# Optimization experiments

Hardware: AMD Instinct MI355X
Metric: run time of the kernel (lower is better)

## Reference

```python
import jax, jax.numpy as jnp
import numpy as np

B, S, H, NH = 8, 1024, 768, 12
I = 3072
HD = H // NH  # 64


def setup_inputs() -> dict:
    key = jax.random.key(0)
    ks = jax.random.split(key, 6)
    w = lambda k, shape: jax.random.normal(k, shape, jnp.float32) * 0.02
    return {
        "x": jax.random.normal(ks[0], (B, S, H), jnp.float32),
        "ln1_g": jnp.ones((H,), jnp.float32),
        "ln1_b": jnp.zeros((H,), jnp.float32),
        "qkv_w": w(ks[1], (H, 3 * H)),
        "qkv_b": jnp.zeros((3 * H,), jnp.float32),
        "proj_w": w(ks[2], (H, H)),
        "proj_b": jnp.zeros((H,), jnp.float32),
        "ln2_g": jnp.ones((H,), jnp.float32),
        "ln2_b": jnp.zeros((H,), jnp.float32),
        "fc1_w": w(ks[3], (H, I)),
        "fc1_b": jnp.zeros((I,), jnp.float32),
        "fc2_w": w(ks[4], (I, H)),
        "fc2_b": jnp.zeros((H,), jnp.float32),
    }


def _layernorm(x, g, b, eps=1e-5):
    m = x.mean(-1, keepdims=True)
    v = x.var(-1, keepdims=True)  # biased variance, matches torch LayerNorm
    return (x - m) * jax.lax.rsqrt(v + eps) * g + b


def _new_gelu(x):
    c = np.float32(np.sqrt(2.0 / np.pi))
    return 0.5 * x * (1.0 + jnp.tanh(c * (x + 0.044715 * x * x * x)))


def reference(x, ln1_g, ln1_b, qkv_w, qkv_b, proj_w, proj_b,
              ln2_g, ln2_b, fc1_w, fc1_b, fc2_w, fc2_b):
    # --- attention sublayer (pre-LN) ---
    h = _layernorm(x, ln1_g, ln1_b)                     # [B,S,H]
    qkv = h @ qkv_w + qkv_b                             # [B,S,3H]
    q, k, v = jnp.split(qkv, 3, axis=-1)
    q = q.reshape(B, S, NH, HD).transpose(0, 2, 1, 3)   # [B,NH,S,HD]
    k = k.reshape(B, S, NH, HD).transpose(0, 2, 1, 3)
    v = v.reshape(B, S, NH, HD).transpose(0, 2, 1, 3)
    scores = jnp.einsum('bhtd,bhsd->bhts', q, k) / np.float32(np.sqrt(HD))
    probs = jax.nn.softmax(scores, axis=-1)             # [B,NH,S,S]
    attn = jnp.einsum('bhts,bhsd->bhtd', probs, v)      # [B,NH,S,HD]
    attn = attn.transpose(0, 2, 1, 3).reshape(B, S, H)
    attn = attn @ proj_w + proj_b
    x = x + attn
    # --- MLP sublayer (pre-LN) ---
    h2 = _layernorm(x, ln2_g, ln2_b)
    m = _new_gelu(h2 @ fc1_w + fc1_b) @ fc2_w + fc2_b
    return x + m
```

## Files before the change

kernel.cpp:

```cpp
#include <hip/hip_runtime.h>
#include <hip/hip_bf16.h>


typedef __attribute__((ext_vector_type(8))) short bf16x8;
typedef __attribute__((ext_vector_type(4))) float f32x4;
typedef const __attribute__((address_space(3))) char* lds_cp;

#define MFMA16(a, b, c) __builtin_amdgcn_mfma_f32_16x16x32_bf16((a), (b), (c), 0, 0, 0)

#define DSR(dst, addr, off) \
    asm volatile("ds_read_b128 %0, %1 offset:" #off : "=v"(dst) : "v"(addr))
#define WAITV4 asm volatile("s_waitcnt vmcnt(4)" ::: "memory")
#define WAITV0 asm volatile("s_waitcnt vmcnt(0)" ::: "memory")
#define WAITLG asm volatile("s_waitcnt lgkmcnt(0)" ::: "memory")
#define SCHEDB __builtin_amdgcn_sched_barrier(0)

__device__ inline short f2bf(float x) {
    __hip_bfloat16 h = __float2bfloat16(x);
    return *reinterpret_cast<short*>(&h);
}

__device__ inline void gload_lds16(const void* g, void* lds) {
    __builtin_amdgcn_global_load_lds(
        (const __attribute__((address_space(1))) unsigned int*)g,
        (__attribute__((address_space(3))) unsigned int*)lds,
        16, 0, 0);
}

__global__ __launch_bounds__(256) void transpose_w(
    const float* __restrict__ W, short* __restrict__ Wt, int K, int N) {
    __shared__ float tile[32][33];
    const int tx = threadIdx.x & 31, ty = threadIdx.x >> 5;
    const int n0 = blockIdx.x * 32, k0 = blockIdx.y * 32;
#pragma unroll
    for (int i = 0; i < 4; ++i)
        tile[ty + i * 8][tx] = W[(size_t)(k0 + ty + i * 8) * N + n0 + tx];
    __syncthreads();
#pragma unroll
    for (int i = 0; i < 4; ++i)
        Wt[(size_t)(n0 + ty + i * 8) * K + k0 + tx] = f2bf(tile[tx][ty + i * 8]);
}

__global__ __launch_bounds__(256) void ln_k(
    const float* __restrict__ x, const float* __restrict__ g,
    const float* __restrict__ b, short* __restrict__ out) {
    const int row = blockIdx.x;
    const int tid = threadIdx.x;
    const float* xr = x + (size_t)row * 768;
    float v[3];
    float s = 0.f, sq = 0.f;
#pragma unroll
    for (int i = 0; i < 3; ++i) {
        v[i] = xr[tid + i * 256];
        s += v[i];
        sq += v[i] * v[i];
    }
#pragma unroll
    for (int off = 32; off >= 1; off >>= 1) {
        s += __shfl_xor(s, off);
        sq += __shfl_xor(sq, off);
    }
    __shared__ float ss[4], ssq[4];
    const int wid = tid >> 6;
    if ((tid & 63) == 0) { ss[wid] = s; ssq[wid] = sq; }
    __syncthreads();
    s = ss[0] + ss[1] + ss[2] + ss[3];
    sq = ssq[0] + ssq[1] + ssq[2] + ssq[3];
    const float mean = s * (1.0f / 768.0f);
    const float var = sq * (1.0f / 768.0f) - mean * mean;
    const float rstd = rsqrtf(var + 1e-5f);
    short* outr = out + (size_t)row * 768;
#pragma unroll
    for (int i = 0; i < 3; ++i) {
        const int c = tid + i * 256;
        outr[c] = f2bf((v[i] - mean) * rstd * g[c] + b[c]);
    }
}

enum { MODE_BF16 = 0, MODE_QKV = 1, MODE_F32RES = 2, MODE_GELU = 3 };

template <int MODE>
__global__ __launch_bounds__(256) void gemm3p(
    const short* __restrict__ A, const short* __restrict__ Wt,
    const float* __restrict__ bias, const float* __restrict__ resid,
    float* __restrict__ outf, short* __restrict__ outh,
    short* __restrict__ Qo, short* __restrict__ Ko, short* __restrict__ Vto,
    int M, int N, int K) {
    __shared__ __attribute__((aligned(128))) short Al[3][4096];
    __shared__ __attribute__((aligned(128))) short Bl[3][4096];
    const int tid = threadIdx.x;
    const int lane = tid & 63;
    const int w = tid >> 6;
    const int wm = w >> 1, wn = w & 1;
    const int m0 = blockIdx.x * 128, n0 = blockIdx.y * 128;

    f32x4 acc[4][4] = {};

    const int srow = tid >> 2;
    const int scol = ((tid & 3) * 8) ^ (((tid >> 2) & 3) << 3);
    const short* Abase = A + (size_t)(m0 + srow) * K + scol;
    const short* Bbase = Wt + (size_t)(n0 + srow) * K + scol;
    const size_t K64 = (size_t)K * 64;
    short* const AlF = &Al[0][0];
    short* const BlF = &Bl[0][0];

    auto stageT = [&](int boS, int k0s) {
        gload_lds16(Abase + k0s,       AlF + boS + w * 512);
        gload_lds16(Abase + K64 + k0s, AlF + boS + 2048 + w * 512);
        gload_lds16(Bbase + k0s,       BlF + boS + w * 512);
        gload_lds16(Bbase + K64 + k0s, BlF + boS + 2048 + w * 512);
    };

    const int lrow = lane & 15;
    const int lcolswz = ((lane >> 4) * 16) ^ ((lane & 3) << 4);
    const int aoff = wm * 4096 + lrow * 64 + lcolswz;
    const int boff = wn * 4096 + lrow * 64 + lcolswz;
    const lds_cp AlB = (lds_cp)AlF;
    const lds_cp BlB = (lds_cp)BlF;

    const int NT = K >> 5;

    stageT(0, 0);
    stageT(4096, 32);
    WAITV4;
    SCHEDB;
    __builtin_amdgcn_s_barrier();

    int bo = 0, bo1 = 8192, bo2 = 16384;
    for (int t = 0; t < NT; ++t) {
        const lds_cp Ab = AlB + (bo + aoff);
        const lds_cp Bb = BlB + (bo + boff);
        bf16x8 av0, av1, av2, av3, bv0, bv1, bv2, bv3;
        DSR(av0, Ab, 0);
        DSR(av1, Ab, 1024);
        DSR(av2, Ab, 2048);
        DSR(av3, Ab, 3072);
        DSR(bv0, Bb, 0);
        DSR(bv1, Bb, 1024);
        DSR(bv2, Bb, 2048);
        DSR(bv3, Bb, 3072);

        int ts = t + 2;
        if (ts > NT - 1) ts = NT - 1;
        stageT(bo2 >> 1, ts << 5);
        WAITV4;
        SCHEDB;
        __builtin_amdgcn_s_barrier();
        WAITLG;
        SCHEDB;

        __builtin_amdgcn_s_setprio(1);
        {
            bf16x8 av[4] = {av0, av1, av2, av3};
            bf16x8 bv[4] = {bv0, bv1, bv2, bv3};
#pragma unroll
            for (int mi = 0; mi < 4; ++mi)
#pragma unroll
                for (int ni = 0; ni < 4; ++ni)
                    acc[mi][ni] = MFMA16(av[mi], bv[ni], acc[mi][ni]);
        }
        __builtin_amdgcn_s_setprio(0);
        __builtin_amdgcn_s_barrier();

        const int tmp = bo; bo = bo1; bo1 = bo2; bo2 = tmp;
    }
    WAITV0;

#pragma unroll
    for (int mi = 0; mi < 4; ++mi) {
#pragma unroll
        for (int ni = 0; ni < 4; ++ni) {
#pragma unroll
            for (int r = 0; r < 4; ++r) {
                const int row = m0 + wm * 64 + mi * 16 + (lane >> 4) * 4 + r;
                const int col = n0 + wn * 64 + ni * 16 + (lane & 15);
                float v = acc[mi][ni][r] + bias[col];
                if constexpr (MODE == MODE_BF16) {
                    outh[(size_t)row * N + col] = f2bf(v);
                } else if constexpr (MODE == MODE_GELU) {
                    const float t = v + 0.044715f * v * v * v;
                    const float gl = 0.5f * v * (1.0f + tanhf(0.7978845608028654f * t));
                    outh[(size_t)row * N + col] = f2bf(gl);
                } else if constexpr (MODE == MODE_F32RES) {
                    outf[(size_t)row * N + col] = v + resid[(size_t)row * N + col];
                } else {
                    const int bb = row >> 10, s = row & 1023;
                    if (col < 768) {
                        const int hh = col >> 6, d = col & 63;
                        Qo[(((size_t)(bb * 12 + hh)) * 1024 + s) * 64 + d] = f2bf(v);
                    } else if (col < 1536) {
                        const int c2 = col - 768;
                        const int hh = c2 >> 6, d = c2 & 63;
                        Ko[(((size_t)(bb * 12 + hh)) * 1024 + s) * 64 + d] = f2bf(v);
                    } else {
                        const int c2 = col - 1536;
                        const int hh = c2 >> 6, d = c2 & 63;
                        Vto[(((size_t)(bb * 12 + hh)) * 64 + d) * 1024 + s] = f2bf(v);
                    }
                }
            }
        }
    }
}

__global__ __launch_bounds__(256) void attn_k(
    const short* __restrict__ Q, const short* __restrict__ Kg,
    const short* __restrict__ Vtg, short* __restrict__ out) {
    __shared__ __attribute__((aligned(128))) short Kl[64 * 80];
    __shared__ __attribute__((aligned(128))) short Vl[64 * 80];
    __shared__ __attribute__((aligned(128))) short Pl[4][16 * 80];
    const int tid = threadIdx.x, lane = tid & 63, w = tid >> 6;
    const int bid = blockIdx.x;
    const int qt = bid & 15, bh = bid >> 4;
    const int b = bh / 12, h = bh % 12;
    const int q0 = qt * 64 + w * 16;

    bf16x8 aq[2];
    const short* Qb = Q + ((size_t)bh * 1024 + q0) * 64;
#pragma unroll
    for (int kk = 0; kk < 2; ++kk)
        aq[kk] = *(const bf16x8*)&Qb[(size_t)(lane & 15) * 64 + kk * 32 + (lane >> 4) * 8];

    float m_run[4], l_run[4];
    f32x4 o[4] = {};
#pragma unroll
    for (int r = 0; r < 4; ++r) { m_run[r] = -1e30f; l_run[r] = 0.f; }

    const short* Kb = Kg + (size_t)bh * 1024 * 64;
    const short* Vb = Vtg + (size_t)bh * 64 * 1024;

    for (int kv0 = 0; kv0 < 1024; kv0 += 64) {
        for (int c = tid; c < 512; c += 256) {
            const int rr = c >> 3, pp = (c & 7) * 8;
            *(bf16x8*)&Kl[rr * 80 + pp] = *(const bf16x8*)&Kb[(size_t)(kv0 + rr) * 64 + pp];
            *(bf16x8*)&Vl[rr * 80 + pp] = *(const bf16x8*)&Vb[(size_t)rr * 1024 + kv0 + pp];
        }
        __syncthreads();

        f32x4 sc[4];
#pragma unroll
        for (int nk = 0; nk < 4; ++nk) {
            const bf16x8 kb0 = *(const bf16x8*)&Kl[(nk * 16 + (lane & 15)) * 80 + (lane >> 4) * 8];
            const bf16x8 kb1 = *(const bf16x8*)&Kl[(nk * 16 + (lane & 15)) * 80 + 32 + (lane >> 4) * 8];
            f32x4 z = {};
            z = MFMA16(aq[0], kb0, z);
            z = MFMA16(aq[1], kb1, z);
            sc[nk] = z * 0.125f;
        }

        float alpha[4], padd[4][4];
#pragma unroll
        for (int r = 0; r < 4; ++r) {
            float ml = fmaxf(fmaxf(sc[0][r], sc[1][r]), fmaxf(sc[2][r], sc[3][r]));
#pragma unroll
            for (int mk = 1; mk <= 8; mk <<= 1) ml = fmaxf(ml, __shfl_xor(ml, mk));
            const float mn = fmaxf(m_run[r], ml);
            alpha[r] = __expf(m_run[r] - mn);
            m_run[r] = mn;
            float rsum = 0.f;
#pragma unroll
            for (int nk = 0; nk < 4; ++nk) {
                padd[nk][r] = __expf(sc[nk][r] - mn);
                rsum += padd[nk][r];
            }
#pragma unroll
            for (int mk = 1; mk <= 8; mk <<= 1) rsum += __shfl_xor(rsum, mk);
            l_run[r] = l_run[r] * alpha[r] + rsum;
#pragma unroll
            for (int dn = 0; dn < 4; ++dn) o[dn][r] *= alpha[r];
        }

#pragma unroll
        for (int nk = 0; nk < 4; ++nk)
#pragma unroll
            for (int r = 0; r < 4; ++r)
                Pl[w][((lane >> 4) * 4 + r) * 80 + nk * 16 + (lane & 15)] = f2bf(padd[nk][r]);
        bf16x8 pa[2];
#pragma unroll
        for (int kk = 0; kk < 2; ++kk)
            pa[kk] = *(const bf16x8*)&Pl[w][(lane & 15) * 80 + kk * 32 + (lane >> 4) * 8];

#pragma unroll
        for (int dn = 0; dn < 4; ++dn) {
            const bf16x8 bv0 = *(const bf16x8*)&Vl[(dn * 16 + (lane & 15)) * 80 + (lane >> 4) * 8];
            const bf16x8 bv1 = *(const bf16x8*)&Vl[(dn * 16 + (lane & 15)) * 80 + 32 + (lane >> 4) * 8];
            o[dn] = MFMA16(pa[0], bv0, o[dn]);
            o[dn] = MFMA16(pa[1], bv1, o[dn]);
        }
        __syncthreads();
    }

#pragma unroll
    for (int dn = 0; dn < 4; ++dn)
#pragma unroll
        for (int r = 0; r < 4; ++r) {
            const int srow = q0 + (lane >> 4) * 4 + r;
            const float v = o[dn][r] / l_run[r];
            out[((size_t)(b * 1024) + srow) * 768 + h * 64 + dn * 16 + (lane & 15)] = f2bf(v);
        }
}

extern "C" void kernel_launch(void* const* d_in, const int* in_sizes, int n_in,
                              void* d_out, int out_size, void* d_ws, size_t ws_size,
                              hipStream_t stream) {
    const float* x      = (const float*)d_in[0];
    const float* ln1_g  = (const float*)d_in[1];
    const float* ln1_b  = (const float*)d_in[2];
    const float* qkv_w  = (const float*)d_in[3];
    const float* qkv_b  = (const float*)d_in[4];
    const float* proj_w = (const float*)d_in[5];
    const float* proj_b = (const float*)d_in[6];
    const float* ln2_g  = (const float*)d_in[7];
    const float* ln2_b  = (const float*)d_in[8];
    const float* fc1_w  = (const float*)d_in[9];
    const float* fc1_b  = (const float*)d_in[10];
    const float* fc2_w  = (const float*)d_in[11];
    const float* fc2_b  = (const float*)d_in[12];
    float* outp = (float*)d_out;

    char* ws = (char*)d_ws;
    size_t off = 0;
    auto alloc = [&](size_t bytes) {
        char* p = ws + off;
        off = (off + bytes + 255) & ~(size_t)255;
        return p;
    };
    short* wt_qkv  = (short*)alloc(2304ull * 768 * 2);
    short* wt_proj = (short*)alloc(768ull * 768 * 2);
    short* wt_fc1  = (short*)alloc(3072ull * 768 * 2);
    short* wt_fc2  = (short*)alloc(768ull * 3072 * 2);
    short* hbuf    = (short*)alloc(8192ull * 768 * 2);
    short* Qb      = (short*)alloc(8192ull * 768 * 2);
    short* Kbuf    = (short*)alloc(8192ull * 768 * 2);
    short* Vtb     = (short*)alloc(8192ull * 768 * 2);
    short* attnb   = (short*)alloc(8192ull * 768 * 2);
    float* x2      = (float*)alloc(8192ull * 768 * 4);
    short* mfc     = Qb;
    (void)ws_size; (void)in_sizes; (void)n_in; (void)out_size;

    transpose_w<<<dim3(2304 / 32, 768 / 32), 256, 0, stream>>>(qkv_w, wt_qkv, 768, 2304);
    transpose_w<<<dim3(768 / 32, 768 / 32), 256, 0, stream>>>(proj_w, wt_proj, 768, 768);
    transpose_w<<<dim3(3072 / 32, 768 / 32), 256, 0, stream>>>(fc1_w, wt_fc1, 768, 3072);
    transpose_w<<<dim3(768 / 32, 3072 / 32), 256, 0, stream>>>(fc2_w, wt_fc2, 3072, 768);

    ln_k<<<8192, 256, 0, stream>>>(x, ln1_g, ln1_b, hbuf);
    gemm3p<MODE_QKV><<<dim3(64, 18), 256, 0, stream>>>(
        hbuf, wt_qkv, qkv_b, nullptr, nullptr, nullptr, Qb, Kbuf, Vtb, 8192, 2304, 768);
    attn_k<<<1536, 256, 0, stream>>>(Qb, Kbuf, Vtb, attnb);
    gemm3p<MODE_F32RES><<<dim3(64, 6), 256, 0, stream>>>(
        attnb, wt_proj, proj_b, x, x2, nullptr, nullptr, nullptr, nullptr, 8192, 768, 768);

    ln_k<<<8192, 256, 0, stream>>>(x2, ln2_g, ln2_b, hbuf);
    gemm3p<MODE_GELU><<<dim3(64, 24), 256, 0, stream>>>(
        hbuf, wt_fc1, fc1_b, nullptr, nullptr, mfc, nullptr, nullptr, nullptr, 8192, 3072, 768);
    gemm3p<MODE_F32RES><<<dim3(64, 6), 256, 0, stream>>>(
        mfc, wt_fc2, fc2_b, x2, outp, nullptr, nullptr, nullptr, nullptr, 8192, 768, 3072);
}
```

Before: 324.5 us.

## Swizzle attention LDS tiles, remap blocks across XCDs, use exp-based GELU

Replaces the padded 80-stride LDS layout for K, V and P tiles in the attention kernel with an unpadded 64-stride layout that uses XOR swizzling to avoid bank conflicts, shrinking LDS use. Block indices are remapped so neighbouring query tiles of the same head land on the same XCD, which should improve L2 reuse of K/V. The GELU epilogue swaps tanhf for an algebraically equivalent sigmoid form built on __expf, which is cheaper but slightly less accurate.

```diff
diff --git a/kernel.cpp b/kernel.cpp
--- a/kernel.cpp
+++ b/kernel.cpp
@@ -178,8 +178,8 @@
                 if constexpr (MODE == MODE_BF16) {
                     outh[(size_t)row * N + col] = f2bf(v);
                 } else if constexpr (MODE == MODE_GELU) {
-                    const float t = v + 0.044715f * v * v * v;
-                    const float gl = 0.5f * v * (1.0f + tanhf(0.7978845608028654f * t));
+                    const float u = 0.7978845608028654f * (v + 0.044715f * v * v * v);
+                    const float gl = v / (1.0f + __expf(-2.0f * u));
                     outh[(size_t)row * N + col] = f2bf(gl);
                 } else if constexpr (MODE == MODE_F32RES) {
                     outf[(size_t)row * N + col] = v + resid[(size_t)row * N + col];
@@ -206,20 +206,22 @@
 __global__ __launch_bounds__(256) void attn_k(
     const short* __restrict__ Q, const short* __restrict__ Kg,
     const short* __restrict__ Vtg, short* __restrict__ out) {
-    __shared__ __attribute__((aligned(128))) short Kl[64 * 80];
-    __shared__ __attribute__((aligned(128))) short Vl[64 * 80];
-    __shared__ __attribute__((aligned(128))) short Pl[4][16 * 80];
+    __shared__ __attribute__((aligned(128))) short Kl[64 * 64];
+    __shared__ __attribute__((aligned(128))) short Vl[64 * 64];
+    __shared__ __attribute__((aligned(128))) short Pl[4][16 * 64];
     const int tid = threadIdx.x, lane = tid & 63, w = tid >> 6;
-    const int bid = blockIdx.x;
-    const int qt = bid & 15, bh = bid >> 4;
+    const int swz = (blockIdx.x & 7) * 192 + (blockIdx.x >> 3);
+    const int qt = swz & 15, bh = swz >> 4;
     const int b = bh / 12, h = bh % 12;
     const int q0 = qt * 64 + w * 16;
 
+    const int l15 = lane & 15, g = lane >> 4;
+
     bf16x8 aq[2];
     const short* Qb = Q + ((size_t)bh * 1024 + q0) * 64;
 #pragma unroll
     for (int kk = 0; kk < 2; ++kk)
-        aq[kk] = *(const bf16x8*)&Qb[(size_t)(lane & 15) * 64 + kk * 32 + (lane >> 4) * 8];
+        aq[kk] = *(const bf16x8*)&Qb[(size_t)l15 * 64 + kk * 32 + g * 8];
 
     float m_run[4], l_run[4];
     f32x4 o[4] = {};
@@ -232,26 +234,29 @@
     for (int kv0 = 0; kv0 < 1024; kv0 += 64) {
         for (int c = tid; c < 512; c += 256) {
             const int rr = c >> 3, pp = (c & 7) * 8;
-            *(bf16x8*)&Kl[rr * 80 + pp] = *(const bf16x8*)&Kb[(size_t)(kv0 + rr) * 64 + pp];
-            *(bf16x8*)&Vl[rr * 80 + pp] = *(const bf16x8*)&Vb[(size_t)rr * 1024 + kv0 + pp];
+            const int sc = pp ^ ((rr & 7) << 3);
+            *(bf16x8*)&Kl[rr * 64 + sc] = *(const bf16x8*)&Kb[(size_t)(kv0 + rr) * 64 + pp];
+            *(bf16x8*)&Vl[rr * 64 + sc] = *(const bf16x8*)&Vb[(size_t)rr * 1024 + kv0 + pp];
         }
         __syncthreads();
 
-        f32x4 sc[4];
+        f32x4 sc4[4];
 #pragma unroll
         for (int nk = 0; nk < 4; ++nk) {
-            const bf16x8 kb0 = *(const bf16x8*)&Kl[(nk * 16 + (lane & 15)) * 80 + (lane >> 4) * 8];
-            const bf16x8 kb1 = *(const bf16x8*)&Kl[(nk * 16 + (lane & 15)) * 80 + 32 + (lane >> 4) * 8];
+            const int R = nk * 16 + l15;
+            const int x = (R & 7) << 3;
+            const bf16x8 kb0 = *(const bf16x8*)&Kl[R * 64 + ((g * 8) ^ x)];
+            const bf16x8 kb1 = *(const bf16x8*)&Kl[R * 64 + ((32 + g * 8) ^ x)];
             f32x4 z = {};
             z = MFMA16(aq[0], kb0, z);
             z = MFMA16(aq[1], kb1, z);
-            sc[nk] = z * 0.125f;
+            sc4[nk] = z * 0.125f;
         }
 
         float alpha[4], padd[4][4];
 #pragma unroll
         for (int r = 0; r < 4; ++r) {
-            float ml = fmaxf(fmaxf(sc[0][r], sc[1][r]), fmaxf(sc[2][r], sc[3][r]));
+            float ml = fmaxf(fmaxf(sc4[0][r], sc4[1][r]), fmaxf(sc4[2][r], sc4[3][r]));
 #pragma unroll
             for (int mk = 1; mk <= 8; mk <<= 1) ml = fmaxf(ml, __shfl_xor(ml, mk));
             const float mn = fmaxf(m_run[r], ml);
@@ -260,7 +265,7 @@
             float rsum = 0.f;
 #pragma unroll
             for (int nk = 0; nk < 4; ++nk) {
-                padd[nk][r] = __expf(sc[nk][r] - mn);
+                padd[nk][r] = __expf(sc4[nk][r] - mn);
                 rsum += padd[nk][r];
             }
 #pragma unroll
@@ -273,17 +278,21 @@
 #pragma unroll
         for (int nk = 0; nk < 4; ++nk)
 #pragma unroll
-            for (int r = 0; r < 4; ++r)
-                Pl[w][((lane >> 4) * 4 + r) * 80 + nk * 16 + (lane & 15)] = f2bf(padd[nk][r]);
+            for (int r = 0; r < 4; ++r) {
+                const int rr = g * 4 + r, cc = nk * 16 + l15;
+                Pl[w][rr * 64 + (cc ^ ((rr & 7) << 3))] = f2bf(padd[nk][r]);
+            }
         bf16x8 pa[2];
 #pragma unroll
         for (int kk = 0; kk < 2; ++kk)
-            pa[kk] = *(const bf16x8*)&Pl[w][(lane & 15) * 80 + kk * 32 + (lane >> 4) * 8];
+            pa[kk] = *(const bf16x8*)&Pl[w][l15 * 64 + ((kk * 32 + g * 8) ^ ((l15 & 7) << 3))];
 
 #pragma unroll
         for (int dn = 0; dn < 4; ++dn) {
-            const bf16x8 bv0 = *(const bf16x8*)&Vl[(dn * 16 + (lane & 15)) * 80 + (lane >> 4) * 8];
-            const bf16x8 bv1 = *(const bf16x8*)&Vl[(dn * 16 + (lane & 15)) * 80 + 32 + (lane >> 4) * 8];
+            const int R = dn * 16 + l15;
+            const int x = (R & 7) << 3;
+            const bf16x8 bv0 = *(const bf16x8*)&Vl[R * 64 + ((g * 8) ^ x)];
+            const bf16x8 bv1 = *(const bf16x8*)&Vl[R * 64 + ((32 + g * 8) ^ x)];
             o[dn] = MFMA16(pa[0], bv0, o[dn]);
             o[dn] = MFMA16(pa[1], bv1, o[dn]);
         }
@@ -294,9 +303,9 @@
     for (int dn = 0; dn < 4; ++dn)
 #pragma unroll
         for (int r = 0; r < 4; ++r) {
-            const int srow = q0 + (lane >> 4) * 4 + r;
+            const int srow = q0 + g * 4 + r;
             const float v = o[dn][r] / l_run[r];
-            out[((size_t)(b * 1024) + srow) * 768 + h * 64 + dn * 16 + (lane & 15)] = f2bf(v);
+            out[((size_t)(b * 1024) + srow) * 768 + h * 64 + dn * 16 + l15] = f2bf(v);
         }
 }
 
```

Result: faster. 310.4 us (-4.4%).
